# Kernel optimization log

Measured on AMD Instinct MI355X. Metric: run time of the kernel, lower is better.

## Reference

```python
import jax, jax.numpy as jnp
import numpy as np
import math

D_MODEL = 768
N_HEADS = 6
HD = D_MODEL // N_HEADS  # 128
RANK = D_MODEL // 4      # 192
B, T = 128, 256


def _rope_tables(T, dim):
    # matches torch: inv = 1/10000**(arange(0,dim,2)/dim); emb = cat([outer(t,inv)]*2, -1)
    inv = 1.0 / (10000.0 ** (jnp.arange(0, dim, 2, dtype=jnp.float32) / dim))
    t = jnp.arange(T, dtype=jnp.float32)
    freqs = jnp.outer(t, inv)                       # [T, dim/2]
    emb = jnp.concatenate([freqs, freqs], axis=-1)  # [T, dim]
    return jnp.cos(emb), jnp.sin(emb)               # each [T, dim]


def _rot(x):
    h = x.shape[-1] // 2
    return jnp.concatenate([-x[..., h:], x[..., :h]], axis=-1)


def setup_inputs() -> dict:
    key = jax.random.key(0)
    ks = jax.random.split(key, 8)
    s_in = 1.0 / math.sqrt(D_MODEL)
    s_r = 1.0 / math.sqrt(RANK)
    inp = {
        'x': jax.random.normal(ks[0], (B, T, D_MODEL), dtype=jnp.float32),
        'qA': jax.random.normal(ks[1], (D_MODEL, RANK), dtype=jnp.float32) * s_in,
        'qB': jax.random.normal(ks[2], (RANK, D_MODEL), dtype=jnp.float32) * s_r,
        'kA': jax.random.normal(ks[3], (D_MODEL, RANK), dtype=jnp.float32) * s_in,
        'kB': jax.random.normal(ks[4], (RANK, D_MODEL), dtype=jnp.float32) * s_r,
        'vA': jax.random.normal(ks[5], (D_MODEL, RANK), dtype=jnp.float32) * s_in,
        'vB': jax.random.normal(ks[6], (RANK, D_MODEL), dtype=jnp.float32) * s_r,
        'o_w': jax.random.normal(ks[7], (D_MODEL, D_MODEL), dtype=jnp.float32) * s_in,
    }
    return inp


def reference(x, qA, qB, kA, kB, vA, vB, o_w):
    Bb, Tt, _ = x.shape
    # low-rank projections: in -> rank -> out, then split heads [B, H, T, hd]
    def proj(A, W):
        h = (x @ A) @ W
        return h.reshape(Bb, Tt, N_HEADS, HD).transpose(0, 2, 1, 3)
    q = proj(qA, qB)
    k = proj(kA, kB)
    v = proj(vA, vB)
    cos, sin = _rope_tables(Tt, HD)  # [T, hd], broadcast over B, H
    q = q * cos + _rot(q) * sin
    k = k * cos + _rot(k) * sin
    att = jnp.einsum('bhqd,bhkd->bhqk', q, k) / math.sqrt(HD)
    causal = jnp.tril(jnp.ones((Tt, Tt), dtype=bool))
    att = jnp.where(causal, att, -jnp.inf)
    att = jax.nn.softmax(att, axis=-1)
    out = jnp.einsum('bhqk,bhkd->bhqd', att, v)          # [B, H, T, hd]
    out = out.transpose(0, 2, 1, 3).reshape(Bb, Tt, D_MODEL)
    return out @ o_w
```

## Files before the change

kernel.cpp:

```cpp
#include <hip/hip_runtime.h>
#include <hip/hip_bf16.h>
#include <stdint.h>

typedef __attribute__((ext_vector_type(8))) short s16x8;
typedef __attribute__((ext_vector_type(4))) float f32x4;

#define D_MODEL 768
#define N_HEADS 6
#define HD 128
#define RANK 192
#define TT 256
#define NROW 32768
#define NK 12
#define QSCL 0.08838834764831845f
#define PSTRIDE 25165824

__device__ inline short f2bf(float f) {
  union { float f; unsigned u; } x; x.f = f;
  unsigned r = x.u + 0x7fffu + ((x.u >> 16) & 1u);
  return (short)(r >> 16);
}
__device__ inline float bf2f(short v) {
  union { unsigned u; float f; } x; x.u = ((unsigned)(unsigned short)v) << 16;
  return x.f;
}
__device__ inline void gload_lds16(const void* g, void* lds) {
  __builtin_amdgcn_global_load_lds(
      (const __attribute__((address_space(1))) unsigned int*)g,
      (__attribute__((address_space(3))) unsigned int*)lds, 16, 0, 0);
}

#define BAR()    asm volatile("s_barrier" ::: "memory")
#define LGKM0()  asm volatile("s_waitcnt lgkmcnt(0)" ::: "memory")
#define WAITVM12() asm volatile("s_waitcnt vmcnt(12)" ::: "memory")
#define WAITVM8()  asm volatile("s_waitcnt vmcnt(8)" ::: "memory")
#define WAITVM4()  asm volatile("s_waitcnt vmcnt(4)" ::: "memory")
#define WAITVM0()  asm volatile("s_waitcnt vmcnt(0)" ::: "memory")
#define SCHB()   __builtin_amdgcn_sched_barrier(0)

__global__ void k_tables(float* __restrict__ cosT, float* __restrict__ sinT) {
  int tid = blockIdx.x * 256 + threadIdx.x;
  int t = tid >> 6, i = tid & 63;
  float inv = powf(10000.0f, -(float)i / 64.0f);
  float ang = (float)t * inv;
  cosT[tid] = cosf(ang);
  sinT[tid] = sinf(ang);
}

__global__ void k_castx(const float* __restrict__ x, short* __restrict__ xb) {
  int t = blockIdx.x * 256 + threadIdx.x;
  const float4* xp = (const float4*)x;
  float4 a = xp[t * 2], b = xp[t * 2 + 1];
  s16x8 o;
  o[0] = f2bf(a.x); o[1] = f2bf(a.y); o[2] = f2bf(a.z); o[3] = f2bf(a.w);
  o[4] = f2bf(b.x); o[5] = f2bf(b.y); o[6] = f2bf(b.z); o[7] = f2bf(b.w);
  *(s16x8*)(xb + (size_t)t * 8) = o;
}

__global__ void k_makew(const float* __restrict__ qA, const float* __restrict__ qB,
                        const float* __restrict__ kA, const float* __restrict__ kB,
                        const float* __restrict__ vA, const float* __restrict__ vB,
                        short* __restrict__ WT) {
  int g = blockIdx.x * 256 + threadIdx.x;
  int n4 = g % 576, kkb = g / 576;
  int part = n4 / 192, nnb = (n4 % 192) * 4;
  const float* A = (part == 0) ? qA : (part == 1) ? kA : vA;
  const float* Bm = (part == 0) ? qB : (part == 1) ? kB : vB;
  float acc[4][4] = {};
  for (int r0 = 0; r0 < RANK; r0 += 4) {
    float4 a4[4], b4[4];
#pragma unroll
    for (int q = 0; q < 4; ++q)
      a4[q] = *(const float4*)&A[(kkb + q * 192) * RANK + r0];
#pragma unroll
    for (int i = 0; i < 4; ++i)
      b4[i] = *(const float4*)&Bm[(r0 + i) * 768 + nnb];
#pragma unroll
    for (int q = 0; q < 4; ++q) {
      const float* aq = (const float*)&a4[q];
#pragma unroll
      for (int i = 0; i < 4; ++i) {
        const float* bi = (const float*)&b4[i];
#pragma unroll
        for (int jn = 0; jn < 4; ++jn)
          acc[q][jn] += aq[i] * bi[jn];
      }
    }
  }
#pragma unroll
  for (int q = 0; q < 4; ++q)
#pragma unroll
    for (int jn = 0; jn < 4; ++jn)
      WT[(size_t)(part * 768 + nnb + jn) * 768 + kkb + q * 192] = f2bf(acc[q][jn]);
}

__global__ void k_wot(const float* __restrict__ ow, short* __restrict__ WT) {
  int g = blockIdx.x * 256 + threadIdx.x;
  int n = g % 768, kk = g / 768;
  WT[(size_t)(2304 + n) * 768 + kk] = f2bf(ow[(size_t)kk * 768 + n]);
}

__device__ inline s16x8 rdfrag(const short* hbase, int rowbyte, int ksl4x, int swz) {
  return *(const s16x8*)((const char*)hbase + rowbyte + (((ksl4x) ^ (swz)) << 4));
}

template <int MODE>
__global__ __launch_bounds__(512, 2) void k_gemm8(const short* __restrict__ A,
                                                  const short* __restrict__ Bt,
                                                  void* __restrict__ Cv, int ldc) {
  extern __shared__ short lds[];
  const int tid = threadIdx.x;
  const int wid = tid >> 6, lane = tid & 63;
  const int l15 = lane & 15, l4 = lane >> 4;
  const int wr = wid >> 2, wc = wid & 3;
  const int swz = l15 & 7;
  const int bid = blockIdx.y * 128 + blockIdx.x;
  const int nper = gridDim.y;
  const int xcd = bid & 7, loc = bid >> 3;
  const int mq = loc / nper;
  const int mt = xcd * 16 + mq;
  const int nt = loc - mq * nper;
  const long mbase = (long)mt * 256;
  const long nbase = (long)nt * 256;

  const int hb0 = wid * 2048 + lane * 16;
  const int hb1 = hb0 + 1024;
  const int r0 = hb0 >> 7, c0 = ((hb0 >> 4) & 7) ^ (r0 & 7);
  const int r1 = hb1 >> 7, c1 = ((hb1 >> 4) & 7) ^ (r1 & 7);
  const int off0 = r0 * 768 + c0 * 8;
  const int off1 = r1 * 768 + c1 * 8;

#define STAGE(G, rowoff, kt, ldsS) do {                                        \
    gload_lds16((G) + (size_t)(rowoff) * 768 + (kt) * 64 + off0,               \
                (char*)(ldsS) + wid * 2048);                                   \
    gload_lds16((G) + (size_t)(rowoff) * 768 + (kt) * 64 + off1,               \
                (char*)(ldsS) + wid * 2048 + 1024);                            \
  } while (0)

#define LDSA(buf, half) (lds + ((buf) * 2 + (half)) * 8192)
#define LDSB(buf, half) (lds + 32768 + ((buf) * 2 + (half)) * 8192)

  f32x4 acc[8][4] = {};

  STAGE(A,  mbase,       0, LDSA(0, 0));
  STAGE(Bt, nbase,       0, LDSB(0, 0));
  STAGE(A,  mbase + 128, 0, LDSA(0, 1));
  STAGE(Bt, nbase + 128, 0, LDSB(0, 1));
  STAGE(A,  mbase,       1, LDSA(1, 0));
  STAGE(Bt, nbase,       1, LDSB(1, 0));
  WAITVM4();
  BAR();

  s16x8 a03[4][2], a47[4][2], b01[2][2], b23[2][2];

#pragma unroll
  for (int kt = 0; kt < NK; ++kt) {
    const int buf = kt & 1, nbuf = buf ^ 1;
    const short* Ab = LDSA(buf, wr);
    const short* Bb = LDSB(buf, (wc >> 1));
    const int browbase = (wc & 1) * 64 * 128;

#pragma unroll
    for (int mf = 0; mf < 4; ++mf)
#pragma unroll
      for (int ks = 0; ks < 2; ++ks)
        a03[mf][ks] = rdfrag(Ab, (mf * 16 + l15) * 128, ks * 4 + l4, swz);
#pragma unroll
    for (int nf = 0; nf < 2; ++nf)
#pragma unroll
      for (int ks = 0; ks < 2; ++ks)
        b01[nf][ks] = rdfrag(Bb, browbase + (nf * 16 + l15) * 128, ks * 4 + l4, swz);
    if (kt + 1 < NK) STAGE(A, mbase + 128, kt + 1, LDSA(nbuf, 1));
    BAR();
    LGKM0();
    __builtin_amdgcn_s_setprio(1);
#pragma unroll
    for (int mf = 0; mf < 4; ++mf)
#pragma unroll
      for (int nf = 0; nf < 2; ++nf)
#pragma unroll
        for (int ks = 0; ks < 2; ++ks)
          acc[mf][nf] = __builtin_amdgcn_mfma_f32_16x16x32_bf16(a03[mf][ks], b01[nf][ks], acc[mf][nf], 0, 0, 0);
    __builtin_amdgcn_s_setprio(0);
    BAR();

#pragma unroll
    for (int mf = 0; mf < 4; ++mf)
#pragma unroll
      for (int ks = 0; ks < 2; ++ks)
        a47[mf][ks] = rdfrag(Ab, ((mf + 4) * 16 + l15) * 128, ks * 4 + l4, swz);
    if (kt + 1 < NK) STAGE(Bt, nbase + 128, kt + 1, LDSB(nbuf, 1));
    BAR();
    LGKM0();
    __builtin_amdgcn_s_setprio(1);
#pragma unroll
    for (int mf = 0; mf < 4; ++mf)
#pragma unroll
      for (int nf = 0; nf < 2; ++nf)
#pragma unroll
        for (int ks = 0; ks < 2; ++ks)
          acc[mf + 4][nf] = __builtin_amdgcn_mfma_f32_16x16x32_bf16(a47[mf][ks], b01[nf][ks], acc[mf + 4][nf], 0, 0, 0);
    __builtin_amdgcn_s_setprio(0);
    BAR();

#pragma unroll
    for (int nf = 0; nf < 2; ++nf)
#pragma unroll
      for (int ks = 0; ks < 2; ++ks)
        b23[nf][ks] = rdfrag(Bb, browbase + ((nf + 2) * 16 + l15) * 128, ks * 4 + l4, swz);
    if (kt + 2 < NK) STAGE(A, mbase, kt + 2, LDSA(buf, 0));
    BAR();
    LGKM0();
    __builtin_amdgcn_s_setprio(1);
#pragma unroll
    for (int mf = 0; mf < 4; ++mf)
#pragma unroll
      for (int nf = 0; nf < 2; ++nf)
#pragma unroll
        for (int ks = 0; ks < 2; ++ks)
          acc[mf][nf + 2] = __builtin_amdgcn_mfma_f32_16x16x32_bf16(a03[mf][ks], b23[nf][ks], acc[mf][nf + 2], 0, 0, 0);
    __builtin_amdgcn_s_setprio(0);
    BAR();

    if (kt + 2 < NK) STAGE(Bt, nbase, kt + 2, LDSB(buf, 0));
    BAR();
    __builtin_amdgcn_s_setprio(1);
#pragma unroll
    for (int mf = 0; mf < 4; ++mf)
#pragma unroll
      for (int nf = 0; nf < 2; ++nf)
#pragma unroll
        for (int ks = 0; ks < 2; ++ks)
          acc[mf + 4][nf + 2] = __builtin_amdgcn_mfma_f32_16x16x32_bf16(a47[mf][ks], b23[nf][ks], acc[mf + 4][nf + 2], 0, 0, 0);
    __builtin_amdgcn_s_setprio(0);
    if (kt < NK - 1) {
      if (kt + 2 < NK) WAITVM4(); else WAITVM0();
      BAR();
    }
  }
#undef STAGE

#pragma unroll
  for (int mf = 0; mf < 8; ++mf)
#pragma unroll
    for (int nf = 0; nf < 4; ++nf) {
      const int col = (int)(nbase + wc * 64 + nf * 16 + l15);
      const int part = col / 768;
      const int wi = col - part * 768;
      const int hh = wi >> 7, dd = wi & 127;
#pragma unroll
      for (int r = 0; r < 4; ++r) {
        long row = mbase + wr * 128 + mf * 16 + l4 * 4 + r;
        if (MODE == 0) {
          ((float*)Cv)[row * ldc + col] = acc[mf][nf][r];
        } else {
          size_t idx = (size_t)part * PSTRIDE +
                       (((size_t)(row >> 8) * 6 + hh) * 256 + (row & 255)) * 128 + dd;
          ((short*)Cv)[idx] = f2bf(acc[mf][nf][r]);
        }
      }
    }
}

__global__ void k_ropek(short* __restrict__ kp, const float* __restrict__ cosT,
                        const float* __restrict__ sinT) {
  int tid = blockIdx.x * 256 + threadIdx.x;
  int bh = tid >> 11, rem = tid & 2047;
  int t = rem >> 3, i8 = (rem & 7) * 8;
  size_t base = ((size_t)bh * 256 + t) * 128 + i8;
  s16x8 a = *(const s16x8*)(kp + base);
  s16x8 b = *(const s16x8*)(kp + base + 64);
  const float4* cp = (const float4*)(cosT + t * 64 + i8);
  const float4* sp = (const float4*)(sinT + t * 64 + i8);
  float4 c04 = cp[0], c14 = cp[1], s04 = sp[0], s14 = sp[1];
  float cs[8] = {c04.x, c04.y, c04.z, c04.w, c14.x, c14.y, c14.z, c14.w};
  float sn[8] = {s04.x, s04.y, s04.z, s04.w, s14.x, s14.y, s14.z, s14.w};
  s16x8 na, nb;
#pragma unroll
  for (int j = 0; j < 8; ++j) {
    float av = bf2f(a[j]), bv = bf2f(b[j]);
    na[j] = f2bf(av * cs[j] - bv * sn[j]);
    nb[j] = f2bf(bv * cs[j] + av * sn[j]);
  }
  *(s16x8*)(kp + base) = na;
  *(s16x8*)(kp + base + 64) = nb;
}

__global__ __launch_bounds__(512) void k_attn(const short* __restrict__ qp,
                                              const short* __restrict__ kp,
                                              const short* __restrict__ vp,
                                              short* __restrict__ attout,
                                              const float* __restrict__ cosT,
                                              const float* __restrict__ sinT) {
  extern __shared__ short smem[];
  short* Vt  = smem + 32768;
  const int tid = threadIdx.x;
  const int wid = tid >> 6, lane = tid & 63;
  const int l15 = lane & 15, l4 = lane >> 4;
  short* PlsW = smem + 40960 + wid * 2048;
  const int bh = blockIdx.x;
  const int b = bh / N_HEADS, h = bh % N_HEADS;
  const long row0 = (long)b * TT;
  const size_t pbase = (size_t)bh * 256 * 128;
  const int d0 = wid * 16;

  s16x8 qf[2][4];
#pragma unroll
  for (int mi = 0; mi < 2; ++mi)
#pragma unroll
    for (int kc = 0; kc < 4; ++kc) {
      int t = wid * 32 + mi * 16 + l15;
      qf[mi][kc] = *(const s16x8*)(qp + pbase + (size_t)t * 128 + kc * 32 + l4 * 8);
    }
#pragma unroll
  for (int mi = 0; mi < 2; ++mi) {
    int t = wid * 32 + mi * 16 + l15;
#pragma unroll
    for (int kc = 0; kc < 2; ++kc) {
      const float4* cp = (const float4*)(cosT + t * 64 + kc * 32 + l4 * 8);
      const float4* sp = (const float4*)(sinT + t * 64 + kc * 32 + l4 * 8);
      float4 c04 = cp[0], c14 = cp[1], s04 = sp[0], s14 = sp[1];
      float cs[8] = {c04.x, c04.y, c04.z, c04.w, c14.x, c14.y, c14.z, c14.w};
      float sn[8] = {s04.x, s04.y, s04.z, s04.w, s14.x, s14.y, s14.z, s14.w};
#pragma unroll
      for (int jj = 0; jj < 8; ++jj) {
        float av = bf2f(qf[mi][kc][jj]);
        float bv = bf2f(qf[mi][kc + 2][jj]);
        qf[mi][kc][jj]     = f2bf((av * cs[jj] - bv * sn[jj]) * QSCL);
        qf[mi][kc + 2][jj] = f2bf((bv * cs[jj] + av * sn[jj]) * QSCL);
      }
    }
  }

#define STAGEK(j_) do {                                                         \
    int bb0_ = wid * 2048 + lane * 16;                                          \
    int r0_ = bb0_ >> 8; int sc0_ = ((bb0_ >> 4) & 15) ^ (r0_ & 7);             \
    gload_lds16(kp + pbase + (size_t)((j_) * 64 + r0_) * 128 + sc0_ * 8,        \
                (char*)(smem + (j_) * 8192) + wid * 2048);                      \
    int bb1_ = bb0_ + 1024;                                                     \
    int r1_ = bb1_ >> 8; int sc1_ = ((bb1_ >> 4) & 15) ^ (r1_ & 7);             \
    gload_lds16(kp + pbase + (size_t)((j_) * 64 + r1_) * 128 + sc1_ * 8,        \
                (char*)(smem + (j_) * 8192) + wid * 2048 + 1024);               \
  } while (0)

#define LOADV(j_, va, vb) do {                                                  \
    const short* vsrc_ = vp + pbase + (size_t)((j_) * 64 + lane) * 128 + d0;    \
    va = *(const s16x8*)vsrc_;                                                  \
    vb = *(const s16x8*)(vsrc_ + 8);                                            \
  } while (0)

  float mst[2][4], lst[2][4];
  f32x4 oacc[2][8];
#pragma unroll
  for (int mi = 0; mi < 2; ++mi)
#pragma unroll
    for (int r = 0; r < 4; ++r) { mst[mi][r] = -1e30f; lst[mi][r] = 0.f; }
#pragma unroll
  for (int mi = 0; mi < 2; ++mi)
#pragma unroll
    for (int nd = 0; nd < 8; ++nd) oacc[mi][nd] = {0.f, 0.f, 0.f, 0.f};

  const int jmax = (wid * 32 + 31) / 64;

  WAITVM0();
  SCHB();
  s16x8 vr[4][2];
  STAGEK(0); SCHB(); LOADV(0, vr[0][0], vr[0][1]); SCHB();
  STAGEK(1); SCHB(); LOADV(1, vr[1][0], vr[1][1]); SCHB();
  STAGEK(2); SCHB(); LOADV(2, vr[2][0], vr[2][1]); SCHB();
  STAGEK(3); SCHB(); LOADV(3, vr[3][0], vr[3][1]); SCHB();

#pragma unroll
  for (int j = 0; j < 4; ++j) {
    if (j == 0) WAITVM12();
    else if (j == 1) WAITVM8();
    else if (j == 2) WAITVM4();
    else WAITVM0();
    SCHB();
    BAR();
#pragma unroll
    for (int e = 0; e < 8; ++e)
      *(short*)((char*)Vt + (d0 + e) * 128 + (((lane >> 3) ^ e) << 4) + (lane & 7) * 2) = vr[j][0][e];
#pragma unroll
    for (int e = 0; e < 8; ++e)
      *(short*)((char*)Vt + (d0 + 8 + e) * 128 + (((lane >> 3) ^ e) << 4) + (lane & 7) * 2) = vr[j][1][e];

    const short* Kb = smem + j * 8192;
    if (j <= jmax) {
      f32x4 sacc[2][4] = {};
#pragma unroll
      for (int kc = 0; kc < 4; ++kc) {
        s16x8 kf[4];
#pragma unroll
        for (int ni = 0; ni < 4; ++ni)
          kf[ni] = *(const s16x8*)((const char*)Kb + (ni * 16 + l15) * 256 +
                                   (((kc * 4 + l4) ^ (l15 & 7)) << 4));
#pragma unroll
        for (int mi = 0; mi < 2; ++mi)
#pragma unroll
          for (int ni = 0; ni < 4; ++ni)
            sacc[mi][ni] = __builtin_amdgcn_mfma_f32_16x16x32_bf16(qf[mi][kc], kf[ni], sacc[mi][ni], 0, 0, 0);
      }
#pragma unroll
      for (int mi = 0; mi < 2; ++mi) {
#pragma unroll
        for (int r = 0; r < 4; ++r) {
          int qr = wid * 32 + mi * 16 + l4 * 4 + r;
          float rm = -1e30f;
#pragma unroll
          for (int ni = 0; ni < 4; ++ni) {
            int kvc = j * 64 + ni * 16 + l15;
            if (kvc > qr) sacc[mi][ni][r] = -1e30f;
            rm = fmaxf(rm, sacc[mi][ni][r]);
          }
#pragma unroll
          for (int d2 = 1; d2 < 16; d2 <<= 1)
            rm = fmaxf(rm, __shfl_xor(rm, d2, 64));
          float mold = mst[mi][r];
          float mnew = fmaxf(mold, rm);
          float alpha = __expf(mold - mnew);
          mst[mi][r] = mnew;
          float rs = 0.f;
#pragma unroll
          for (int ni = 0; ni < 4; ++ni) {
            float p = __expf(sacc[mi][ni][r] - mnew);
            sacc[mi][ni][r] = p;
            rs += p;
          }
#pragma unroll
          for (int d2 = 1; d2 < 16; d2 <<= 1)
            rs += __shfl_xor(rs, d2, 64);
          lst[mi][r] = lst[mi][r] * alpha + rs;
#pragma unroll
          for (int nd = 0; nd < 8; ++nd)
            oacc[mi][nd][r] *= alpha;
        }
      }
#pragma unroll
      for (int mi = 0; mi < 2; ++mi)
#pragma unroll
        for (int ni = 0; ni < 4; ++ni)
#pragma unroll
          for (int r = 0; r < 4; ++r) {
            int prow = mi * 16 + l4 * 4 + r;
            int pcp = (ni * 2 + (l15 >> 3)) ^ (prow & 7);
            *(short*)((char*)PlsW + prow * 128 + (pcp << 4) + (l15 & 7) * 2) =
                f2bf(sacc[mi][ni][r]);
          }
    }
    LGKM0();
    BAR();
    SCHB();
    if (j <= jmax) {
#pragma unroll
      for (int kc2 = 0; kc2 < 2; ++kc2) {
        s16x8 pa[2];
#pragma unroll
        for (int mi = 0; mi < 2; ++mi)
          pa[mi] = *(const s16x8*)((const char*)PlsW + (mi * 16 + l15) * 128 +
                                   (((kc2 * 4 + l4) ^ (l15 & 7)) << 4));
#pragma unroll
        for (int nd = 0; nd < 8; ++nd) {
          s16x8 vf = *(const s16x8*)((const char*)Vt + (nd * 16 + l15) * 128 +
                                     (((kc2 * 4 + l4) ^ (l15 & 7)) << 4));
#pragma unroll
          for (int mi = 0; mi < 2; ++mi)
            oacc[mi][nd] = __builtin_amdgcn_mfma_f32_16x16x32_bf16(pa[mi], vf, oacc[mi][nd], 0, 0, 0);
        }
      }
    }
  }
#undef STAGEK
#undef LOADV
#pragma unroll
  for (int mi = 0; mi < 2; ++mi)
#pragma unroll
    for (int nd = 0; nd < 8; ++nd)
#pragma unroll
      for (int r = 0; r < 4; ++r) {
        long row = row0 + wid * 32 + mi * 16 + l4 * 4 + r;
        int col = h * HD + nd * 16 + l15;
        attout[row * D_MODEL + col] = f2bf(oacc[mi][nd][r] / lst[mi][r]);
      }
}

extern "C" void kernel_launch(void* const* d_in, const int* in_sizes, int n_in,
                              void* d_out, int out_size, void* d_ws, size_t ws_size,
                              hipStream_t stream) {
  const float* x  = (const float*)d_in[0];
  const float* qA = (const float*)d_in[1];
  const float* qB = (const float*)d_in[2];
  const float* kA = (const float*)d_in[3];
  const float* kB = (const float*)d_in[4];
  const float* vA = (const float*)d_in[5];
  const float* vB = (const float*)d_in[6];
  const float* ow = (const float*)d_in[7];

  char* ws = (char*)d_ws;
  short* qkvp  = (short*)ws;
  short* qp    = qkvp;
  short* kp    = qkvp + (size_t)PSTRIDE;
  short* vp    = qkvp + (size_t)2 * PSTRIDE;
  short* xb    = (short*)(ws + 150994944);
  short* WT    = (short*)(ws + 201326592);
  float* cosT  = (float*)(ws + 206045184);
  float* sinT  = (float*)(ws + 206110720);
  short* attout = xb;

  hipFuncSetAttribute((const void*)k_gemm8<2>,
                      hipFuncAttributeMaxDynamicSharedMemorySize, 131072);
  hipFuncSetAttribute((const void*)k_gemm8<0>,
                      hipFuncAttributeMaxDynamicSharedMemorySize, 131072);
  hipFuncSetAttribute((const void*)k_attn,
                      hipFuncAttributeMaxDynamicSharedMemorySize, 114688);

  k_tables<<<64, 256, 0, stream>>>(cosT, sinT);
  k_castx<<<12288, 256, 0, stream>>>(x, xb);
  k_makew<<<432, 256, 0, stream>>>(qA, qB, kA, kB, vA, vB, WT);
  k_wot<<<2304, 256, 0, stream>>>(ow, WT);
  k_gemm8<2><<<dim3(128, 9), 512, 131072, stream>>>(xb, WT, (void*)qkvp, 0);
  k_ropek<<<6144, 256, 0, stream>>>(kp, cosT, sinT);
  k_attn<<<768, 512, 114688, stream>>>(qp, kp, vp, attout, cosT, sinT);
  k_gemm8<0><<<dim3(128, 3), 512, 131072, stream>>>(attout, WT + (size_t)2304 * 768, d_out, 768);
}
```

Measured before the change: 356.7 us.

## Stage all V tiles into LDS upfront and drop per-tile block barriers

The attention kernel now issues all K staging and V loads at once, waits for all of them, and transposes every V tile into its own LDS region before a single barrier. The per-tile loop then runs only up to each wave's causal limit, with no block-wide barriers inside it, since each wave reads only its private P buffer and read-only K/V. This removes the per-iteration barriers and the wasted loop passes for masked tiles. In exchange LDS use grows from 112KB to 160KB per block, and the load pipelining that overlapped early tiles with later loads is lost.

Measured after the change: 366.3 us. 2.7% more time.

```diff
diff --git a/kernel.cpp b/kernel.cpp
--- a/kernel.cpp
+++ b/kernel.cpp
@@ -32,10 +32,8 @@
 
 #define BAR()    asm volatile("s_barrier" ::: "memory")
 #define LGKM0()  asm volatile("s_waitcnt lgkmcnt(0)" ::: "memory")
-#define WAITVM12() asm volatile("s_waitcnt vmcnt(12)" ::: "memory")
-#define WAITVM8()  asm volatile("s_waitcnt vmcnt(8)" ::: "memory")
-#define WAITVM4()  asm volatile("s_waitcnt vmcnt(4)" ::: "memory")
-#define WAITVM0()  asm volatile("s_waitcnt vmcnt(0)" ::: "memory")
+#define WAITVM4() asm volatile("s_waitcnt vmcnt(4)" ::: "memory")
+#define WAITVM0() asm volatile("s_waitcnt vmcnt(0)" ::: "memory")
 #define SCHB()   __builtin_amdgcn_sched_barrier(0)
 
 __global__ void k_tables(float* __restrict__ cosT, float* __restrict__ sinT) {
@@ -293,11 +291,10 @@
                                               const float* __restrict__ cosT,
                                               const float* __restrict__ sinT) {
   extern __shared__ short smem[];
-  short* Vt  = smem + 32768;
   const int tid = threadIdx.x;
   const int wid = tid >> 6, lane = tid & 63;
   const int l15 = lane & 15, l4 = lane >> 4;
-  short* PlsW = smem + 40960 + wid * 2048;
+  short* PlsW = smem + 65536 + wid * 2048;
   const int bh = blockIdx.x;
   const int b = bh / N_HEADS, h = bh % N_HEADS;
   const long row0 = (long)b * TT;
@@ -362,111 +359,106 @@
 
   const int jmax = (wid * 32 + 31) / 64;
 
+  s16x8 vr[4][2];
+  STAGEK(0); STAGEK(1); STAGEK(2); STAGEK(3);
+  LOADV(0, vr[0][0], vr[0][1]);
+  LOADV(1, vr[1][0], vr[1][1]);
+  LOADV(2, vr[2][0], vr[2][1]);
+  LOADV(3, vr[3][0], vr[3][1]);
   WAITVM0();
   SCHB();
-  s16x8 vr[4][2];
-  STAGEK(0); SCHB(); LOADV(0, vr[0][0], vr[0][1]); SCHB();
-  STAGEK(1); SCHB(); LOADV(1, vr[1][0], vr[1][1]); SCHB();
-  STAGEK(2); SCHB(); LOADV(2, vr[2][0], vr[2][1]); SCHB();
-  STAGEK(3); SCHB(); LOADV(3, vr[3][0], vr[3][1]); SCHB();
-
-#pragma unroll
-  for (int j = 0; j < 4; ++j) {
-    if (j == 0) WAITVM12();
-    else if (j == 1) WAITVM8();
-    else if (j == 2) WAITVM4();
-    else WAITVM0();
+#pragma unroll
+  for (int jt = 0; jt < 4; ++jt) {
+    char* Vtj = (char*)(smem + 32768 + jt * 8192);
+#pragma unroll
+    for (int e = 0; e < 8; ++e)
+      *(short*)(Vtj + (d0 + e) * 128 + (((lane >> 3) ^ e) << 4) + (lane & 7) * 2) = vr[jt][0][e];
+#pragma unroll
+    for (int e = 0; e < 8; ++e)
+      *(short*)(Vtj + (d0 + 8 + e) * 128 + (((lane >> 3) ^ e) << 4) + (lane & 7) * 2) = vr[jt][1][e];
+  }
+  LGKM0();
+  BAR();
+
+  for (int j = 0; j <= jmax; ++j) {
+    const short* Kb  = smem + j * 8192;
+    const char*  Vtj = (const char*)(smem + 32768 + j * 8192);
+    f32x4 sacc[2][4] = {};
+#pragma unroll
+    for (int kc = 0; kc < 4; ++kc) {
+      s16x8 kf[4];
+#pragma unroll
+      for (int ni = 0; ni < 4; ++ni)
+        kf[ni] = *(const s16x8*)((const char*)Kb + (ni * 16 + l15) * 256 +
+                                 (((kc * 4 + l4) ^ (l15 & 7)) << 4));
+#pragma unroll
+      for (int mi = 0; mi < 2; ++mi)
+#pragma unroll
+        for (int ni = 0; ni < 4; ++ni)
+          sacc[mi][ni] = __builtin_amdgcn_mfma_f32_16x16x32_bf16(qf[mi][kc], kf[ni], sacc[mi][ni], 0, 0, 0);
+    }
+#pragma unroll
+    for (int mi = 0; mi < 2; ++mi) {
+#pragma unroll
+      for (int r = 0; r < 4; ++r) {
+        int qr = wid * 32 + mi * 16 + l4 * 4 + r;
+        float rm = -1e30f;
+#pragma unroll
+        for (int ni = 0; ni < 4; ++ni) {
+          int kvc = j * 64 + ni * 16 + l15;
+          if (kvc > qr) sacc[mi][ni][r] = -1e30f;
+          rm = fmaxf(rm, sacc[mi][ni][r]);
+        }
+#pragma unroll
+        for (int d2 = 1; d2 < 16; d2 <<= 1)
+          rm = fmaxf(rm, __shfl_xor(rm, d2, 64));
+        float mold = mst[mi][r];
+        float mnew = fmaxf(mold, rm);
+        float alpha = __expf(mold - mnew);
+        mst[mi][r] = mnew;
+        float rs = 0.f;
+#pragma unroll
+        for (int ni = 0; ni < 4; ++ni) {
+          float p = __expf(sacc[mi][ni][r] - mnew);
+          sacc[mi][ni][r] = p;
+          rs += p;
+        }
+#pragma unroll
+        for (int d2 = 1; d2 < 16; d2 <<= 1)
+          rs += __shfl_xor(rs, d2, 64);
+        lst[mi][r] = lst[mi][r] * alpha + rs;
+#pragma unroll
+        for (int nd = 0; nd < 8; ++nd)
+          oacc[mi][nd][r] *= alpha;
+      }
+    }
+#pragma unroll
+    for (int mi = 0; mi < 2; ++mi)
+#pragma unroll
+      for (int ni = 0; ni < 4; ++ni)
+#pragma unroll
+        for (int r = 0; r < 4; ++r) {
+          int prow = mi * 16 + l4 * 4 + r;
+          int pcp = (ni * 2 + (l15 >> 3)) ^ (prow & 7);
+          *(short*)((char*)PlsW + prow * 128 + (pcp << 4) + (l15 & 7) * 2) =
+              f2bf(sacc[mi][ni][r]);
+        }
+    LGKM0();
     SCHB();
-    BAR();
-#pragma unroll
-    for (int e = 0; e < 8; ++e)
-      *(short*)((char*)Vt + (d0 + e) * 128 + (((lane >> 3) ^ e) << 4) + (lane & 7) * 2) = vr[j][0][e];
-#pragma unroll
-    for (int e = 0; e < 8; ++e)
-      *(short*)((char*)Vt + (d0 + 8 + e) * 128 + (((lane >> 3) ^ e) << 4) + (lane & 7) * 2) = vr[j][1][e];
-
-    const short* Kb = smem + j * 8192;
-    if (j <= jmax) {
-      f32x4 sacc[2][4] = {};
-#pragma unroll
-      for (int kc = 0; kc < 4; ++kc) {
-        s16x8 kf[4];
-#pragma unroll
-        for (int ni = 0; ni < 4; ++ni)
-          kf[ni] = *(const s16x8*)((const char*)Kb + (ni * 16 + l15) * 256 +
-                                   (((kc * 4 + l4) ^ (l15 & 7)) << 4));
+#pragma unroll
+    for (int kc2 = 0; kc2 < 2; ++kc2) {
+      s16x8 pa[2];
+#pragma unroll
+      for (int mi = 0; mi < 2; ++mi)
+        pa[mi] = *(const s16x8*)((const char*)PlsW + (mi * 16 + l15) * 128 +
+                                 (((kc2 * 4 + l4) ^ (l15 & 7)) << 4));
+#pragma unroll
+      for (int nd = 0; nd < 8; ++nd) {
+        s16x8 vf = *(const s16x8*)(Vtj + (nd * 16 + l15) * 128 +
+                                   (((kc2 * 4 + l4) ^ (l15 & 7)) << 4));
 #pragma unroll
         for (int mi = 0; mi < 2; ++mi)
-#pragma unroll
-          for (int ni = 0; ni < 4; ++ni)
-            sacc[mi][ni] = __builtin_amdgcn_mfma_f32_16x16x32_bf16(qf[mi][kc], kf[ni], sacc[mi][ni], 0, 0, 0);
-      }
-#pragma unroll
-      for (int mi = 0; mi < 2; ++mi) {
-#pragma unroll
-        for (int r = 0; r < 4; ++r) {
-          int qr = wid * 32 + mi * 16 + l4 * 4 + r;
-          float rm = -1e30f;
-#pragma unroll
-          for (int ni = 0; ni < 4; ++ni) {
-            int kvc = j * 64 + ni * 16 + l15;
-            if (kvc > qr) sacc[mi][ni][r] = -1e30f;
-            rm = fmaxf(rm, sacc[mi][ni][r]);
-          }
-#pragma unroll
-          for (int d2 = 1; d2 < 16; d2 <<= 1)
-            rm = fmaxf(rm, __shfl_xor(rm, d2, 64));
-          float mold = mst[mi][r];
-          float mnew = fmaxf(mold, rm);
-          float alpha = __expf(mold - mnew);
-          mst[mi][r] = mnew;
-          float rs = 0.f;
-#pragma unroll
-          for (int ni = 0; ni < 4; ++ni) {
-            float p = __expf(sacc[mi][ni][r] - mnew);
-            sacc[mi][ni][r] = p;
-            rs += p;
-          }
-#pragma unroll
-          for (int d2 = 1; d2 < 16; d2 <<= 1)
-            rs += __shfl_xor(rs, d2, 64);
-          lst[mi][r] = lst[mi][r] * alpha + rs;
-#pragma unroll
-          for (int nd = 0; nd < 8; ++nd)
-            oacc[mi][nd][r] *= alpha;
-        }
-      }
-#pragma unroll
-      for (int mi = 0; mi < 2; ++mi)
-#pragma unroll
-        for (int ni = 0; ni < 4; ++ni)
-#pragma unroll
-          for (int r = 0; r < 4; ++r) {
-            int prow = mi * 16 + l4 * 4 + r;
-            int pcp = (ni * 2 + (l15 >> 3)) ^ (prow & 7);
-            *(short*)((char*)PlsW + prow * 128 + (pcp << 4) + (l15 & 7) * 2) =
-                f2bf(sacc[mi][ni][r]);
-          }
-    }
-    LGKM0();
-    BAR();
-    SCHB();
-    if (j <= jmax) {
-#pragma unroll
-      for (int kc2 = 0; kc2 < 2; ++kc2) {
-        s16x8 pa[2];
-#pragma unroll
-        for (int mi = 0; mi < 2; ++mi)
-          pa[mi] = *(const s16x8*)((const char*)PlsW + (mi * 16 + l15) * 128 +
-                                   (((kc2 * 4 + l4) ^ (l15 & 7)) << 4));
-#pragma unroll
-        for (int nd = 0; nd < 8; ++nd) {
-          s16x8 vf = *(const s16x8*)((const char*)Vt + (nd * 16 + l15) * 128 +
-                                     (((kc2 * 4 + l4) ^ (l15 & 7)) << 4));
-#pragma unroll
-          for (int mi = 0; mi < 2; ++mi)
-            oacc[mi][nd] = __builtin_amdgcn_mfma_f32_16x16x32_bf16(pa[mi], vf, oacc[mi][nd], 0, 0, 0);
-        }
+          oacc[mi][nd] = __builtin_amdgcn_mfma_f32_16x16x32_bf16(pa[mi], vf, oacc[mi][nd], 0, 0, 0);
       }
     }
   }
@@ -512,7 +504,7 @@
   hipFuncSetAttribute((const void*)k_gemm8<0>,
                       hipFuncAttributeMaxDynamicSharedMemorySize, 131072);
   hipFuncSetAttribute((const void*)k_attn,
-                      hipFuncAttributeMaxDynamicSharedMemorySize, 114688);
+                      hipFuncAttributeMaxDynamicSharedMemorySize, 163840);
 
   k_tables<<<64, 256, 0, stream>>>(cosT, sinT);
   k_castx<<<12288, 256, 0, stream>>>(x, xb);
@@ -520,6 +512,6 @@
   k_wot<<<2304, 256, 0, stream>>>(ow, WT);
   k_gemm8<2><<<dim3(128, 9), 512, 131072, stream>>>(xb, WT, (void*)qkvp, 0);
   k_ropek<<<6144, 256, 0, stream>>>(kp, cosT, sinT);
-  k_attn<<<768, 512, 114688, stream>>>(qp, kp, vp, attout, cosT, sinT);
+  k_attn<<<768, 512, 163840, stream>>>(qp, kp, vp, attout, cosT, sinT);
   k_gemm8<0><<<dim3(128, 3), 512, 131072, stream>>>(attout, WT + (size_t)2304 * 768, d_out, 768);
 }
```
